# Optimization experiments

Measured on AMD Instinct MI355X. Metric: run time of the kernel, lower is better.

The kernel has to match this reference:

```python
import jax, jax.numpy as jnp
import numpy as np

DIM = 3          # algebra dimension (3D Clifford algebra Cl(3,0))
NB = 2 ** DIM    # 8 blades
C_IN, C_OUT = 4, 4
K = 3            # conv kernel size
S = 48           # spatial size (== mask_size)
B = 4            # batch size
HID = 128


def _build_algebra():
    """Cayley table of Cl(3,0) with blades ordered by (grade, bitmask), and the
    path matrix M[p, bj, bk] = sum_bi cayley[bi,bj,bk] restricted to grade-triple p."""
    n = NB
    blades = sorted(range(n), key=lambda b: (bin(b).count('1'), b))
    idx = {b: i for i, b in enumerate(blades)}
    grades = np.array([bin(b).count('1') for b in blades])
    cay = np.zeros((n, n, n), dtype=np.float32)
    for a in range(n):
        for b in range(n):
            s = 1
            t = a >> 1
            while t:
                s *= (-1) ** bin(t & b).count('1')
                t >>= 1
            cay[idx[a], idx[b], idx[a ^ b]] = s  # Euclidean metric: no extra signs
    ng = DIM + 1
    path_id = -np.ones((ng, ng, ng), dtype=int)
    p = 0
    for gi in range(ng):
        for gj in range(ng):
            for gk in range(ng):
                if np.any(cay[np.ix_(np.where(grades == gi)[0], np.where(grades == gj)[0], np.where(grades == gk)[0])] != 0):
                    path_id[gi, gj, gk] = p
                    p += 1
    P = p  # == product_paths_sum == 20 for Cl(3,0)
    M = np.zeros((P, n, n), dtype=np.float32)
    for i in range(n):
        for j in range(n):
            for k in range(n):
                c = cay[i, j, k]
                if c != 0.0:
                    M[path_id[grades[i], grades[j], grades[k]], j, k] += c
    return M, P

CAYLEY_M, P = _build_algebra()


def _circular_mask(ks):
    c = (ks - 1) / 2.0
    zz, yy, xx = np.ogrid[:ks, :ks, :ks]
    d = np.sqrt((xx - c) ** 2 + (yy - c) ** 2 + (zz - c) ** 2)
    return (d <= c).astype(np.float32)


def _rel_pos_mv():
    """Kernel-grid offsets embedded as grade-1 multivectors: (K^3, NB)."""
    ax = np.linspace(-1.0, 1.0, K).astype(np.float32)
    gx, gy, gz = np.meshgrid(ax, ax, ax, indexing='ij')
    pos = np.stack([gx, gy, gz], -1).reshape(-1, DIM)
    mv = np.zeros((K ** DIM, NB), dtype=np.float32)
    mv[:, 1:1 + DIM] = pos  # grade-1 blade slots are indices 1..3
    return mv


def setup_inputs() -> dict:
    key = jax.random.key(0)
    ks = jax.random.split(key, 4)
    x = jax.random.normal(ks[0], (B, C_IN, S, S, S, NB), jnp.float32)
    w0 = jax.random.normal(ks[1], (2 * NB, HID), jnp.float32) / np.sqrt(2 * NB)
    w1 = jax.random.normal(ks[2], (HID, HID), jnp.float32) / np.sqrt(HID)
    w2 = jax.random.normal(ks[3], (HID, C_OUT * C_IN * P), jnp.float32) / np.sqrt(HID)
    return {
        'x': x,
        'w0': w0, 'b0': jnp.zeros((HID,), jnp.float32),
        'w1': w1, 'b1': jnp.zeros((HID,), jnp.float32),
        'w2': w2, 'b2': jnp.zeros((C_OUT * C_IN * P,), jnp.float32),
        'bias_param': jnp.zeros((C_OUT, 1, 1, 1, 1), jnp.float32),
    }


def reference(x, w0, b0, w1, b1, w2, b2, bias_param):
    # 1) masked global pooling -> per-sample per-blade condition (B, NB)
    mask = jnp.asarray(_circular_mask(S))
    cond = jnp.einsum('bcxyzn,xyz->bn', x, mask) / (mask.sum() * C_IN)

    # 2) per-sample dynamic kernel generation (vmapped kernel network)
    rel = jnp.asarray(_rel_pos_mv())               # (X, NB), X = K^3
    X = K ** DIM
    feat = jnp.concatenate([
        jnp.broadcast_to(rel[None], (B, X, NB)),
        jnp.broadcast_to(cond[:, None, :], (B, X, NB)),
    ], axis=-1)                                     # (B, X, 2*NB)
    h = jax.nn.gelu(feat @ w0 + b0)
    h = jax.nn.gelu(h @ w1 + b1)
    w = (h @ w2 + b2).reshape(B, X, C_OUT, C_IN, P)  # per-path geometric-product weights

    # 3) assemble blade-level kernel via sparse Cayley contraction
    M = jnp.asarray(CAYLEY_M)                       # (P, NB_in_blade, NB_out_blade)
    ker = jnp.einsum('bxoip,pjk->bokijx', w, M)     # (B, o, bk, i, bj, X)
    kernels = ker.reshape(B * C_OUT * NB, C_IN * NB, K, K, K)

    # 4) grouped conv: one kernel bank per sample (feature_group_count = B)
    inp = jnp.transpose(x, (0, 1, 5, 2, 3, 4)).reshape(1, B * C_IN * NB, S, S, S)
    out = jax.lax.conv_general_dilated(
        inp, kernels, window_strides=(1, 1, 1), padding='SAME',
        dimension_numbers=('NCDHW', 'OIDHW', 'NCDHW'), feature_group_count=B)
    out = out.reshape(B, C_OUT, NB, S, S, S)
    out = jnp.transpose(out, (0, 1, 3, 4, 5, 2))    # (B, c_out, S,S,S, NB)

    # 5) multivector bias embedded at blade dims (0,)
    bias = jnp.zeros((C_OUT, 1, 1, 1, NB), x.dtype).at[..., 0:1].set(bias_param)
    return out + bias
```

## Files before the change

kernel.cpp:

```cpp
#include <hip/hip_runtime.h>
#include <cmath>

#define SS 48
#define S3 110592
#define NB 8
#define CIN 4
#define COUT 4
#define HID 128
#define XT 27
#define NP 20
#define BATCH 4
#define PD 50
#define PD2 2500
#define PD3 125000
#define SLABV 648
#define SLABS 5184

typedef __attribute__((ext_vector_type(8))) short short8;
typedef __attribute__((ext_vector_type(4))) float f32x4;

struct Tables {
    int   pid[64];
    float sgn[64];
};

__device__ __forceinline__ unsigned short bf16_rne(float f) {
    union { float f; unsigned u; } c; c.f = f;
    unsigned r = c.u + 0x7FFF + ((c.u >> 16) & 1);
    return (unsigned short)(r >> 16);
}

__device__ __forceinline__ float gelu_tanh(float v) {
    const float c = 0.7978845608028654f;
    float u = c * (v + 0.044715f * v * v * v);
    return 0.5f * v * (1.0f + tanhf(u));
}

__global__ __launch_bounds__(256)
void pack_cond_kernel(const float* __restrict__ x, unsigned short* __restrict__ xb,
                      float* __restrict__ partial) {
    int b  = blockIdx.y;
    int pv = blockIdx.x * 256 + threadIdx.x;
    __shared__ float sacc[8];
    if (threadIdx.x < 8) sacc[threadIdx.x] = 0.0f;
    __syncthreads();
    float acc[8];
#pragma unroll
    for (int n = 0; n < 8; ++n) acc[n] = 0.0f;
    if (pv < PD3) {
        int zp = pv / PD2, rem = pv % PD2, yp = rem / PD, xp = rem % PD;
        int z = zp - 1, y = yp - 1, xx = xp - 1;
        unsigned short ob[32];
        bool interior = (unsigned)z < 48u && (unsigned)y < 48u && (unsigned)xx < 48u;
        if (interior) {
            int v = (z * 48 + y) * 48 + xx;
            float vals[32];
#pragma unroll
            for (int i = 0; i < 4; ++i) {
                const f32x4* p = (const f32x4*)(x + (((size_t)(b * 4 + i)) * S3 + v) * 8);
                f32x4 a = p[0], c4 = p[1];
                vals[i * 8 + 0] = a[0];  vals[i * 8 + 1] = a[1];
                vals[i * 8 + 2] = a[2];  vals[i * 8 + 3] = a[3];
                vals[i * 8 + 4] = c4[0]; vals[i * 8 + 5] = c4[1];
                vals[i * 8 + 6] = c4[2]; vals[i * 8 + 7] = c4[3];
            }
            int dx = 2 * xx - 47, dy = 2 * y - 47, dz = 2 * z - 47;
            if (dx * dx + dy * dy + dz * dz <= 2209) {
#pragma unroll
                for (int n = 0; n < 8; ++n)
                    acc[n] = vals[n] + vals[8 + n] + vals[16 + n] + vals[24 + n];
            }
#pragma unroll
            for (int k = 0; k < 32; ++k) ob[k] = bf16_rne(vals[k]);
        } else {
#pragma unroll
            for (int k = 0; k < 32; ++k) ob[k] = 0;
        }
        short8* dst = (short8*)(xb + ((size_t)b * PD3 + pv) * 32);
#pragma unroll
        for (int q = 0; q < 4; ++q) {
            short8 s;
#pragma unroll
            for (int e = 0; e < 8; ++e) s[e] = (short)ob[q * 8 + e];
            dst[q] = s;
        }
    }
#pragma unroll
    for (int n = 0; n < 8; ++n) {
        float a = acc[n];
        for (int off = 32; off; off >>= 1) a += __shfl_down(a, off);
        if ((threadIdx.x & 63) == 0) atomicAdd(&sacc[n], a);
    }
    __syncthreads();
    if (threadIdx.x < 8)
        partial[((size_t)b * 512 + blockIdx.x) * 8 + threadIdx.x] = sacc[threadIdx.x];
}

__global__ __launch_bounds__(256)
void cond_reduce(const float* __restrict__ partial, float* __restrict__ cond) {
    int b = blockIdx.x, t = threadIdx.x;
    __shared__ float red[32][8];
    int ch = t & 7, seg = t >> 3;
    float s = 0.0f;
    for (int j = seg; j < 489; j += 32)
        s += partial[((size_t)b * 512 + j) * 8 + ch];
    red[seg][ch] = s;
    __syncthreads();
    if (t < 8) {
        float s2 = 0.0f;
#pragma unroll
        for (int q = 0; q < 32; ++q) s2 += red[q][t];
        cond[b * 8 + t] = s2;
    }
}

__global__ __launch_bounds__(128)
void mlp12(const float* __restrict__ cond,
           const float* __restrict__ w0, const float* __restrict__ b0,
           const float* __restrict__ w1, const float* __restrict__ b1,
           float* __restrict__ h2out, float inv_norm) {
    int bx = blockIdx.x;
    int b = bx / XT, tap = bx % XT;
    int t = threadIdx.x;
    __shared__ float feat[16];
    __shared__ float h1[HID];
    if (t < 16) {
        float v = 0.0f;
        if (t < 8) {
            if (t == 1) v = (float)(tap / 9) - 1.0f;
            else if (t == 2) v = (float)((tap / 3) % 3) - 1.0f;
            else if (t == 3) v = (float)(tap % 3) - 1.0f;
        } else {
            v = cond[b * 8 + (t - 8)] * inv_norm;
        }
        feat[t] = v;
    }
    __syncthreads();
    float s = b0[t];
#pragma unroll
    for (int k = 0; k < 16; ++k) s += feat[k] * w0[k * HID + t];
    h1[t] = gelu_tanh(s);
    __syncthreads();
    float a0 = b1[t], a1 = 0.0f, a2 = 0.0f, a3 = 0.0f;
#pragma unroll
    for (int k = 0; k < HID; k += 4) {
        a0 += h1[k + 0] * w1[(k + 0) * HID + t];
        a1 += h1[k + 1] * w1[(k + 1) * HID + t];
        a2 += h1[k + 2] * w1[(k + 2) * HID + t];
        a3 += h1[k + 3] * w1[(k + 3) * HID + t];
    }
    h2out[(size_t)bx * HID + t] = gelu_tanh((a0 + a1) + (a2 + a3));
}

__global__ __launch_bounds__(320)
void mlp3(const float* __restrict__ h2in, const float* __restrict__ w2,
          const float* __restrict__ b2, unsigned short* __restrict__ wb, Tables tb) {
    int bx = blockIdx.x;
    int b = bx / XT, tap = bx % XT;
    int t = threadIdx.x;
    __shared__ float h2[HID];
    __shared__ float wrow[320];
    if (t < HID) h2[t] = h2in[(size_t)bx * HID + t];
    __syncthreads();
    float a0 = b2[t], a1 = 0.0f, a2 = 0.0f, a3 = 0.0f;
#pragma unroll
    for (int k = 0; k < HID; k += 4) {
        a0 += h2[k + 0] * w2[(size_t)(k + 0) * 320 + t];
        a1 += h2[k + 1] * w2[(size_t)(k + 1) * 320 + t];
        a2 += h2[k + 2] * w2[(size_t)(k + 2) * 320 + t];
        a3 += h2[k + 3] * w2[(size_t)(k + 3) * 320 + t];
    }
    wrow[t] = (a0 + a1) + (a2 + a3);
    __syncthreads();
    if (t < 128) {
        int m = t >> 2, cq = t & 3;
        int o = m >> 3, bk = m & 7;
        short8 sv;
#pragma unroll
        for (int e = 0; e < 8; ++e) {
            int c = cq * 8 + e;
            int i = c >> 3, bj = c & 7, jk = bj * 8 + bk;
            sv[e] = (short)bf16_rne(tb.sgn[jk] * wrow[o * 80 + i * 20 + tb.pid[jk]]);
        }
        int g  = (tap / 9) * 3 + (tap % 3);
        int ky = (tap % 9) / 3;
        int half = m >> 4, mm = m & 15;
        size_t tile = (size_t)(b * 27 + g * 3 + ky) * 1024;
        *(short8*)(wb + tile + half * 512 + (mm + cq * 16) * 8) = sv;
    }
}

__global__ __launch_bounds__(256, 3)
void conv_lds(const unsigned short* __restrict__ xb, const unsigned short* __restrict__ wb,
              const float* __restrict__ bias, float* __restrict__ out) {
    __shared__ __align__(16) short lds[4 * SLABS];
    int b  = blockIdx.y;
    int bx = blockIdx.x;
    int tx = bx % 3, ty = (bx / 3) % 12, tz = bx / 36;
    int X0 = tx * 16, Y0 = ty * 4, Z0 = tz * 4;
    int tid = threadIdx.x, lane = tid & 63, wave = tid >> 6;

    const unsigned short* xsrc = xb + (size_t)b * PD3 * 32 +
        ((size_t)Z0 * PD2 + (size_t)Y0 * PD + X0) * 32 + wave * 8;
#pragma unroll
    for (int k = 0; k < 11; ++k) {
        int h0 = k * 64, h = h0 + lane;
        if (h < SLABV) {
            int hz = h / 108, rem = h % 108, hy = rem / 18, hx = rem % 18;
            __builtin_amdgcn_global_load_lds(
                (const unsigned int*)(xsrc + ((size_t)hz * PD2 + hy * PD + hx) * 32),
                (unsigned int*)&lds[wave * SLABS + h0 * 8], 16, 0, 0);
        }
    }

    int col = lane & 15, kl = lane >> 4;
    int mh = wave >> 1, zp = (wave & 1) * 2;

    const unsigned short* wgl = wb + (size_t)b * 27648 + mh * 512 + lane * 8;
    short8 wcur[9], wnxt[9];
#pragma unroll
    for (int t9 = 0; t9 < 9; ++t9)
        wcur[t9] = *(const short8*)(wgl + (size_t)t9 * 1024);
    __syncthreads();

    f32x4 acc[2][4];
#pragma unroll
    for (int s = 0; s < 2; ++s)
#pragma unroll
        for (int r = 0; r < 4; ++r)
#pragma unroll
            for (int e = 0; e < 4; ++e) acc[s][r][e] = 0.0f;

#pragma unroll
    for (int kz = 0; kz < 3; ++kz) {
        if (kz < 2) {
#pragma unroll
            for (int t9 = 0; t9 < 9; ++t9)
                wnxt[t9] = *(const short8*)(wgl + (size_t)((kz + 1) * 9 + t9) * 1024);
        }
#pragma unroll
        for (int kx = 0; kx < 3; ++kx) {
#pragma unroll
            for (int s = 0; s < 2; ++s) {
                const short* lb = &lds[kl * SLABS + ((zp + s + kz) * 108 + col + kx) * 8];
                short8 bfv[6];
#pragma unroll
                for (int u = 0; u < 6; ++u)
                    bfv[u] = *(const short8*)(lb + u * 144);
#pragma unroll
                for (int ky = 0; ky < 3; ++ky) {
                    short8 a = wcur[kx * 3 + ky];
#pragma unroll
                    for (int r = 0; r < 4; ++r)
                        acc[s][r] = __builtin_amdgcn_mfma_f32_16x16x32_bf16(a, bfv[r + ky], acc[s][r], 0, 0, 0);
                }
            }
        }
        if (kz < 2) {
#pragma unroll
            for (int t9 = 0; t9 < 9; ++t9) wcur[t9] = wnxt[t9];
        }
    }

    int xc = X0 + col;
    int m0 = kl * 4 + mh * 16;
    int o = m0 >> 3, bk0 = m0 & 7;
    float bi = (bk0 == 0) ? bias[o] : 0.0f;
#pragma unroll
    for (int s = 0; s < 2; ++s) {
        int z = Z0 + zp + s;
#pragma unroll
        for (int r = 0; r < 4; ++r) {
            int y = Y0 + r;
            int vox = (z * 48 + y) * 48 + xc;
            f32x4 v = acc[s][r];
            v[0] += bi;
            *(f32x4*)(out + (((size_t)(b * 4 + o)) * S3 + vox) * 8 + bk0) = v;
        }
    }
}

static inline int pc_host(int v) { return __builtin_popcount(v); }

extern "C" void kernel_launch(void* const* d_in, const int* in_sizes, int n_in,
                              void* d_out, int out_size, void* d_ws, size_t ws_size,
                              hipStream_t stream) {
    const float* x    = (const float*)d_in[0];
    const float* w0   = (const float*)d_in[1];
    const float* b0   = (const float*)d_in[2];
    const float* w1   = (const float*)d_in[3];
    const float* b1   = (const float*)d_in[4];
    const float* w2   = (const float*)d_in[5];
    const float* b2   = (const float*)d_in[6];
    const float* bias = (const float*)d_in[7];
    float* out = (float*)d_out;

    float* ws      = (float*)d_ws;
    float* partial = ws;
    float* cond    = ws + 16384;
    float* h2buf   = ws + 16448;
    unsigned short* wbb = (unsigned short*)(ws + 30272);
    unsigned short* xb  = wbb + 110592;

    int cnt = 0;
    for (int z = 0; z < SS; ++z) {
        int dz = 2 * z - 47;
        for (int y = 0; y < SS; ++y) {
            int dy = 2 * y - 47;
            for (int xx = 0; xx < SS; ++xx) {
                int dx = 2 * xx - 47;
                if (dx * dx + dy * dy + dz * dz <= 2209) ++cnt;
            }
        }
    }
    float inv_norm = 1.0f / ((float)cnt * (float)CIN);

    int pidtab[4][4][4];
    {
        bool ex[4][4][4] = {};
        for (int A = 0; A < 8; ++A)
            for (int B = 0; B < 8; ++B)
                ex[pc_host(A)][pc_host(B)][pc_host(A ^ B)] = true;
        int p = 0;
        for (int gi = 0; gi < 4; ++gi)
            for (int gj = 0; gj < 4; ++gj)
                for (int gk = 0; gk < 4; ++gk)
                    pidtab[gi][gj][gk] = ex[gi][gj][gk] ? p++ : -1;
    }
    static const int blades[8] = {0, 1, 2, 4, 3, 5, 6, 7};
    Tables tb;
    for (int bj = 0; bj < 8; ++bj) {
        for (int bk = 0; bk < 8; ++bk) {
            int bmj = blades[bj], bmk = blades[bk];
            int bma = bmj ^ bmk;
            int sgn = 1, t = bma >> 1;
            while (t) {
                if (pc_host(t & bmj) & 1) sgn = -sgn;
                t >>= 1;
            }
            tb.sgn[bj * 8 + bk] = (float)sgn;
            tb.pid[bj * 8 + bk] = pidtab[pc_host(bma)][pc_host(bmj)][pc_host(bmk)];
        }
    }

    pack_cond_kernel<<<dim3(489, BATCH), dim3(256), 0, stream>>>(x, xb, partial);
    cond_reduce<<<dim3(BATCH), dim3(256), 0, stream>>>(partial, cond);
    mlp12<<<dim3(BATCH * XT), dim3(128), 0, stream>>>(cond, w0, b0, w1, b1, h2buf, inv_norm);
    mlp3<<<dim3(BATCH * XT), dim3(320), 0, stream>>>(h2buf, w2, b2, wbb, tb);
    conv_lds<<<dim3(432, BATCH), dim3(256), 0, stream>>>(xb, wbb, bias, out);
}
```

Baseline: 69.29 us.

## Fuse cond reduction and MLP into one kernel; remap conv waves to z-slices

Merges cond_reduce, mlp12 and mlp3 into one kernel, in which each block redundantly reduces the partial sums and runs all three MLP layers. This removes two launches and the global round-trips for cond and h2. In the conv kernel, each wave now owns one z-slice and computes both M halves. The B fragments read from LDS are reused across two MFMA streams, at the cost of loading both weight halves per kz without the previous double-buffer prefetch.

```diff
diff --git a/kernel.cpp b/kernel.cpp
--- a/kernel.cpp
+++ b/kernel.cpp
@@ -96,81 +96,70 @@
         partial[((size_t)b * 512 + blockIdx.x) * 8 + threadIdx.x] = sacc[threadIdx.x];
 }
 
-__global__ __launch_bounds__(256)
-void cond_reduce(const float* __restrict__ partial, float* __restrict__ cond) {
-    int b = blockIdx.x, t = threadIdx.x;
-    __shared__ float red[32][8];
-    int ch = t & 7, seg = t >> 3;
-    float s = 0.0f;
-    for (int j = seg; j < 489; j += 32)
-        s += partial[((size_t)b * 512 + j) * 8 + ch];
-    red[seg][ch] = s;
-    __syncthreads();
-    if (t < 8) {
-        float s2 = 0.0f;
-#pragma unroll
-        for (int q = 0; q < 32; ++q) s2 += red[q][t];
-        cond[b * 8 + t] = s2;
-    }
-}
-
-__global__ __launch_bounds__(128)
-void mlp12(const float* __restrict__ cond,
-           const float* __restrict__ w0, const float* __restrict__ b0,
-           const float* __restrict__ w1, const float* __restrict__ b1,
-           float* __restrict__ h2out, float inv_norm) {
+__global__ __launch_bounds__(320)
+void mlp_fused(const float* __restrict__ partial,
+               const float* __restrict__ w0, const float* __restrict__ b0,
+               const float* __restrict__ w1, const float* __restrict__ b1,
+               const float* __restrict__ w2, const float* __restrict__ b2,
+               unsigned short* __restrict__ wb, float inv_norm, Tables tb) {
     int bx = blockIdx.x;
     int b = bx / XT, tap = bx % XT;
     int t = threadIdx.x;
+    __shared__ float red[40][8];
     __shared__ float feat[16];
     __shared__ float h1[HID];
-    if (t < 16) {
-        float v = 0.0f;
-        if (t < 8) {
-            if (t == 1) v = (float)(tap / 9) - 1.0f;
-            else if (t == 2) v = (float)((tap / 3) % 3) - 1.0f;
-            else if (t == 3) v = (float)(tap % 3) - 1.0f;
-        } else {
-            v = cond[b * 8 + (t - 8)] * inv_norm;
-        }
-        feat[t] = v;
-    }
-    __syncthreads();
-    float s = b0[t];
-#pragma unroll
-    for (int k = 0; k < 16; ++k) s += feat[k] * w0[k * HID + t];
-    h1[t] = gelu_tanh(s);
-    __syncthreads();
-    float a0 = b1[t], a1 = 0.0f, a2 = 0.0f, a3 = 0.0f;
-#pragma unroll
-    for (int k = 0; k < HID; k += 4) {
-        a0 += h1[k + 0] * w1[(k + 0) * HID + t];
-        a1 += h1[k + 1] * w1[(k + 1) * HID + t];
-        a2 += h1[k + 2] * w1[(k + 2) * HID + t];
-        a3 += h1[k + 3] * w1[(k + 3) * HID + t];
-    }
-    h2out[(size_t)bx * HID + t] = gelu_tanh((a0 + a1) + (a2 + a3));
-}
-
-__global__ __launch_bounds__(320)
-void mlp3(const float* __restrict__ h2in, const float* __restrict__ w2,
-          const float* __restrict__ b2, unsigned short* __restrict__ wb, Tables tb) {
-    int bx = blockIdx.x;
-    int b = bx / XT, tap = bx % XT;
-    int t = threadIdx.x;
     __shared__ float h2[HID];
     __shared__ float wrow[320];
-    if (t < HID) h2[t] = h2in[(size_t)bx * HID + t];
-    __syncthreads();
-    float a0 = b2[t], a1 = 0.0f, a2 = 0.0f, a3 = 0.0f;
-#pragma unroll
-    for (int k = 0; k < HID; k += 4) {
-        a0 += h2[k + 0] * w2[(size_t)(k + 0) * 320 + t];
-        a1 += h2[k + 1] * w2[(size_t)(k + 1) * 320 + t];
-        a2 += h2[k + 2] * w2[(size_t)(k + 2) * 320 + t];
-        a3 += h2[k + 3] * w2[(size_t)(k + 3) * 320 + t];
-    }
-    wrow[t] = (a0 + a1) + (a2 + a3);
+    {
+        int ch = t & 7, seg = t >> 3;
+        float s = 0.0f;
+        for (int j = seg; j < 489; j += 40)
+            s += partial[((size_t)b * 512 + j) * 8 + ch];
+        red[seg][ch] = s;
+    }
+    __syncthreads();
+    if (t < 8) {
+        float s2 = 0.0f;
+#pragma unroll
+        for (int q = 0; q < 40; ++q) s2 += red[q][t];
+        feat[8 + t] = s2 * inv_norm;
+        float v = 0.0f;
+        if (t == 1) v = (float)(tap / 9) - 1.0f;
+        else if (t == 2) v = (float)((tap / 3) % 3) - 1.0f;
+        else if (t == 3) v = (float)(tap % 3) - 1.0f;
+        feat[t] = v;
+    }
+    __syncthreads();
+    if (t < 128) {
+        float s = b0[t];
+#pragma unroll
+        for (int k = 0; k < 16; ++k) s += feat[k] * w0[k * HID + t];
+        h1[t] = gelu_tanh(s);
+    }
+    __syncthreads();
+    if (t < 128) {
+        float a0 = b1[t], a1 = 0.0f, a2 = 0.0f, a3 = 0.0f;
+#pragma unroll
+        for (int k = 0; k < HID; k += 4) {
+            a0 += h1[k + 0] * w1[(k + 0) * HID + t];
+            a1 += h1[k + 1] * w1[(k + 1) * HID + t];
+            a2 += h1[k + 2] * w1[(k + 2) * HID + t];
+            a3 += h1[k + 3] * w1[(k + 3) * HID + t];
+        }
+        h2[t] = gelu_tanh((a0 + a1) + (a2 + a3));
+    }
+    __syncthreads();
+    {
+        float a0 = b2[t], a1 = 0.0f, a2 = 0.0f, a3 = 0.0f;
+#pragma unroll
+        for (int k = 0; k < HID; k += 4) {
+            a0 += h2[k + 0] * w2[(size_t)(k + 0) * 320 + t];
+            a1 += h2[k + 1] * w2[(size_t)(k + 1) * 320 + t];
+            a2 += h2[k + 2] * w2[(size_t)(k + 2) * 320 + t];
+            a3 += h2[k + 3] * w2[(size_t)(k + 3) * 320 + t];
+        }
+        wrow[t] = (a0 + a1) + (a2 + a3);
+    }
     __syncthreads();
     if (t < 128) {
         int m = t >> 2, cq = t & 3;
@@ -214,66 +203,55 @@
     }
 
     int col = lane & 15, kl = lane >> 4;
-    int mh = wave >> 1, zp = (wave & 1) * 2;
-
-    const unsigned short* wgl = wb + (size_t)b * 27648 + mh * 512 + lane * 8;
-    short8 wcur[9], wnxt[9];
-#pragma unroll
-    for (int t9 = 0; t9 < 9; ++t9)
-        wcur[t9] = *(const short8*)(wgl + (size_t)t9 * 1024);
+    const unsigned short* wgl = wb + (size_t)b * 27648 + lane * 8;
     __syncthreads();
 
     f32x4 acc[2][4];
 #pragma unroll
-    for (int s = 0; s < 2; ++s)
+    for (int mh = 0; mh < 2; ++mh)
 #pragma unroll
         for (int r = 0; r < 4; ++r)
 #pragma unroll
-            for (int e = 0; e < 4; ++e) acc[s][r][e] = 0.0f;
+            for (int e = 0; e < 4; ++e) acc[mh][r][e] = 0.0f;
 
 #pragma unroll
     for (int kz = 0; kz < 3; ++kz) {
-        if (kz < 2) {
+        short8 wr[2][9];
+#pragma unroll
+        for (int mh = 0; mh < 2; ++mh)
 #pragma unroll
             for (int t9 = 0; t9 < 9; ++t9)
-                wnxt[t9] = *(const short8*)(wgl + (size_t)((kz + 1) * 9 + t9) * 1024);
-        }
+                wr[mh][t9] = *(const short8*)(wgl + (size_t)(kz * 9 + t9) * 1024 + mh * 512);
 #pragma unroll
         for (int kx = 0; kx < 3; ++kx) {
-#pragma unroll
-            for (int s = 0; s < 2; ++s) {
-                const short* lb = &lds[kl * SLABS + ((zp + s + kz) * 108 + col + kx) * 8];
-                short8 bfv[6];
-#pragma unroll
-                for (int u = 0; u < 6; ++u)
-                    bfv[u] = *(const short8*)(lb + u * 144);
-#pragma unroll
-                for (int ky = 0; ky < 3; ++ky) {
-                    short8 a = wcur[kx * 3 + ky];
-#pragma unroll
-                    for (int r = 0; r < 4; ++r)
-                        acc[s][r] = __builtin_amdgcn_mfma_f32_16x16x32_bf16(a, bfv[r + ky], acc[s][r], 0, 0, 0);
+            const short* lb = &lds[kl * SLABS + ((wave + kz) * 108 + col + kx) * 8];
+            short8 bfv[6];
+#pragma unroll
+            for (int u = 0; u < 6; ++u)
+                bfv[u] = *(const short8*)(lb + u * 144);
+#pragma unroll
+            for (int ky = 0; ky < 3; ++ky) {
+#pragma unroll
+                for (int r = 0; r < 4; ++r) {
+                    acc[0][r] = __builtin_amdgcn_mfma_f32_16x16x32_bf16(wr[0][kx * 3 + ky], bfv[r + ky], acc[0][r], 0, 0, 0);
+                    acc[1][r] = __builtin_amdgcn_mfma_f32_16x16x32_bf16(wr[1][kx * 3 + ky], bfv[r + ky], acc[1][r], 0, 0, 0);
                 }
             }
         }
-        if (kz < 2) {
-#pragma unroll
-            for (int t9 = 0; t9 < 9; ++t9) wcur[t9] = wnxt[t9];
-        }
     }
 
     int xc = X0 + col;
-    int m0 = kl * 4 + mh * 16;
-    int o = m0 >> 3, bk0 = m0 & 7;
-    float bi = (bk0 == 0) ? bias[o] : 0.0f;
-#pragma unroll
-    for (int s = 0; s < 2; ++s) {
-        int z = Z0 + zp + s;
+    int z  = Z0 + wave;
+#pragma unroll
+    for (int mh = 0; mh < 2; ++mh) {
+        int m0 = kl * 4 + mh * 16;
+        int o = m0 >> 3, bk0 = m0 & 7;
+        float bi = (bk0 == 0) ? bias[o] : 0.0f;
 #pragma unroll
         for (int r = 0; r < 4; ++r) {
             int y = Y0 + r;
             int vox = (z * 48 + y) * 48 + xc;
-            f32x4 v = acc[s][r];
+            f32x4 v = acc[mh][r];
             v[0] += bi;
             *(f32x4*)(out + (((size_t)(b * 4 + o)) * S3 + vox) * 8 + bk0) = v;
         }
@@ -297,8 +275,6 @@
 
     float* ws      = (float*)d_ws;
     float* partial = ws;
-    float* cond    = ws + 16384;
-    float* h2buf   = ws + 16448;
     unsigned short* wbb = (unsigned short*)(ws + 30272);
     unsigned short* xb  = wbb + 110592;
 
@@ -344,8 +320,7 @@
     }
 
     pack_cond_kernel<<<dim3(489, BATCH), dim3(256), 0, stream>>>(x, xb, partial);
-    cond_reduce<<<dim3(BATCH), dim3(256), 0, stream>>>(partial, cond);
-    mlp12<<<dim3(BATCH * XT), dim3(128), 0, stream>>>(cond, w0, b0, w1, b1, h2buf, inv_norm);
-    mlp3<<<dim3(BATCH * XT), dim3(320), 0, stream>>>(h2buf, w2, b2, wbb, tb);
+    mlp_fused<<<dim3(BATCH * XT), dim3(320), 0, stream>>>(partial, w0, b0, w1, b1, w2, b2,
+                                                          wbb, inv_norm, tb);
     conv_lds<<<dim3(432, BATCH), dim3(256), 0, stream>>>(xb, wbb, bias, out);
 }
```

Result: slower. 72.14 us (+4.1%).
